# Kernel tuning notes

Hardware: AMD Instinct MI355X
Metric: run time of the kernel (lower is better)

Reference implementation:

```python
import jax, jax.numpy as jnp
import numpy as np

NEG_INF = -1e9


def setup_inputs() -> dict:
    key = jax.random.key(0)
    k1, k2, k3, k4, k5, k6 = jax.random.split(key, 6)
    B, P, N, C, H = 32, 512, 64, 9, 128
    polylines = jax.random.normal(k1, (B, P, N, C), dtype=jnp.float32)
    polylines_mask = jax.random.uniform(k2, (B, P, N)) > 0.1
    # MLP params (Linear(C,H) -> ReLU -> Linear(H,H)), torch-style init scale
    W1 = jax.random.uniform(k3, (C, H), minval=-1.0, maxval=1.0) / jnp.sqrt(C)
    b1 = jax.random.uniform(k4, (H,), minval=-1.0, maxval=1.0) / jnp.sqrt(C)
    W2 = jax.random.uniform(k5, (H, H), minval=-1.0, maxval=1.0) / jnp.sqrt(H)
    b2 = jax.random.uniform(k6, (H,), minval=-1.0, maxval=1.0) / jnp.sqrt(H)
    return {"polylines": polylines, "polylines_mask": polylines_mask,
            "W1": W1, "b1": b1, "W2": W2, "b2": b2}


def reference(polylines, polylines_mask, W1, b1, W2, b2):
    # Point MLP applied to all points (invalid ones are overwritten below,
    # identical math to the torch masked-gather version).
    h = jax.nn.relu(jnp.einsum('bpnc,ch->bpnh', polylines, W1) + b1)
    feat = jnp.einsum('bpnh,hd->bpnd', h, W2) + b2  # [B,P,N,H]
    feat = jnp.where(polylines_mask[..., None], feat, NEG_INF)
    pooled = jnp.max(feat, axis=2)  # [B,P,H]
    # Polylines with no valid points pooled to NEG_INF -> zero them out.
    any_valid = jnp.any(polylines_mask, axis=2)  # [B,P]
    return jnp.where(any_valid[..., None], pooled, 0.0)
```

## Files before the change

### kernel.cpp

```cpp
#include <hip/hip_runtime.h>


using bf16x8 = __attribute__((ext_vector_type(8))) short;
using f32x4  = __attribute__((ext_vector_type(4))) float;

#define MFMA32(A,B,C) __builtin_amdgcn_mfma_f32_16x16x32_bf16((A),(B),(C),0,0,0)

__device__ __forceinline__ f32x4 vmax4(f32x4 a, f32x4 b) {
  return __builtin_elementwise_max(a, b);
}

__device__ __forceinline__ unsigned short f2bf(float f) {
  union { float f; unsigned int u; } v; v.f = f;
  unsigned int r = v.u + 0x7fffu + ((v.u >> 16) & 1u);
  return (unsigned short)(r >> 16);
}

__device__ __forceinline__ unsigned int pack_bf2(float a, float b) {
  union { float f; unsigned int u; } ua, ub; ua.f = a; ub.f = b;
  return __builtin_amdgcn_perm(ub.u + 0x8000u, ua.u + 0x8000u, 0x07060302u);
}

__global__ void prep1(const float* __restrict__ W1, const float* __restrict__ W2,
                      const void* __restrict__ mask,
                      unsigned short* __restrict__ w1sw, unsigned short* __restrict__ w2sw,
                      int* __restrict__ flag) {
  int b = blockIdx.x, t = threadIdx.x;
  if (b == 0) {
    __shared__ int cnt;
    if (t == 0) cnt = 0;
    __syncthreads();
    const unsigned char* mb = (const unsigned char*)mask;
    int local = 0;
    for (int i = t * 16; i < t * 16 + 16; i++) local += (mb[i] != 0) ? 1 : 0;
    atomicAdd(&cnt, local);
    __syncthreads();
    if (t == 0) *flag = (cnt > 2800) ? 1 : 0;
  } else if (b <= 2) {
    int e = (b - 1) * 256 + t;
    int lane = e & 63, grp = e >> 6;
    int li = lane & 15, q = lane >> 4;
    int h = grp * 16 + li;
    int c0 = q * 8;
    #pragma unroll
    for (int j = 0; j < 8; j++) {
      int c = c0 + j;
      w1sw[e * 8 + j] = f2bf((c < 9) ? W1[c * 128 + h] : 0.f);
    }
  } else {
    int e = (b - 3) * 256 + t;
    if (e < 2048) {
      int lane = e & 63, grp = e >> 6;
      int wr = grp >> 4, sub = grp & 15;
      int ks = sub >> 2, td = sub & 3;
      int li = lane & 15, q = lane >> 4;
      int d = wr * 64 + td * 16 + li;
      int h0 = ks * 32 + q * 8;
      #pragma unroll
      for (int j = 0; j < 8; j++)
        w2sw[e * 8 + j] = f2bf(W2[(h0 + j) * 128 + d]);
    }
  }
}

__global__ __launch_bounds__(256, 4) void poly_main_k(
    const float* __restrict__ X, const void* __restrict__ mask,
    const float* __restrict__ b1g, const float* __restrict__ b2g,
    const unsigned short* __restrict__ w1sw, const unsigned short* __restrict__ w2sw,
    const int* __restrict__ flagp, float* __restrict__ out)
{
  __shared__ __align__(16) unsigned char smem[32768];
  float*          Xs = (float*)smem;
  unsigned short* Hb = (unsigned short*)smem;
  float*          P  = (float*)smem;

  const int tid  = threadIdx.x;
  const int lane = tid & 63;
  const int w    = tid >> 6;
  const int wr   = w >> 1, wc = w & 1;
  const int li   = lane & 15, q = lane >> 4;

  float mf[4];
  {
    int flag = *flagp;
    long long mb = (long long)blockIdx.x * 128 + wc * 64 + li;
    if (flag) {
      const unsigned char* mp = (const unsigned char*)mask;
      #pragma unroll
      for (int tm = 0; tm < 4; tm++) mf[tm] = mp[mb + tm * 16] ? 0.f : -4e9f;
    } else {
      const int* mp = (const int*)mask;
      #pragma unroll
      for (int tm = 0; tm < 4; tm++) mf[tm] = mp[mb + tm * 16] ? 0.f : -4e9f;
    }
  }

  {
    const f32x4* xg = (const f32x4*)(X + (long long)blockIdx.x * 1152);
    f32x4* xl = (f32x4*)Xs;
    xl[tid] = xg[tid];
    if (tid < 32) xl[tid + 256] = xg[tid + 256];
  }
  __syncthreads();

  bf16x8 bx[4];
  #pragma unroll
  for (int tm = 0; tm < 4; tm++) {
    int m = wc * 64 + tm * 16 + li;
    const float* xr = Xs + m * 9;
    union { bf16x8 v; unsigned int u[4]; } uu;
    uu.u[0] = uu.u[1] = uu.u[2] = uu.u[3] = 0u;
    if (q == 0) {
      uu.u[0] = pack_bf2(xr[0], xr[1]); uu.u[1] = pack_bf2(xr[2], xr[3]);
      uu.u[2] = pack_bf2(xr[4], xr[5]); uu.u[3] = pack_bf2(xr[6], xr[7]);
    } else if (q == 1) {
      uu.u[0] = pack_bf2(xr[8], 0.f);
    }
    bx[tm] = uu.v;
  }
  __syncthreads();

  #pragma unroll
  for (int th = 0; th < 4; th++) {
    bf16x8 a1 = *(const bf16x8*)(w1sw + ((wr * 4 + th) * 64 + lane) * 8);
    f32x4 bv = *(const f32x4*)(b1g + wr * 64 + th * 16 + q * 4);
    f32x4 acc[4];
    #pragma unroll
    for (int tm = 0; tm < 4; tm++) acc[tm] = bv;
    #pragma unroll
    for (int tm = 0; tm < 4; tm++) acc[tm] = MFMA32(a1, bx[tm], acc[tm]);
    #pragma unroll
    for (int tm = 0; tm < 4; tm++) {
      int m = wc * 64 + tm * 16 + li;
      f32x4 v = vmax4(acc[tm], f32x4{0.f, 0.f, 0.f, 0.f});
      uint2 hv;
      hv.x = pack_bf2(v[0], v[1]);
      hv.y = pack_bf2(v[2], v[3]);
      int chunk = (wr * 8 + th * 2 + (q >> 1)) ^ li;
      *(uint2*)(Hb + m * 128 + chunk * 8 + (q & 1) * 4) = hv;
    }
  }
  __syncthreads();

  f32x4 pooled[4];
  #pragma unroll
  for (int tm = 0; tm < 4; tm++) {
    int m = wc * 64 + tm * 16 + li;
    f32x4 acc[4];
    #pragma unroll
    for (int td = 0; td < 4; td++) acc[td] = f32x4{0.f, 0.f, 0.f, 0.f};
    #pragma unroll
    for (int ks = 0; ks < 4; ks++) {
      int chunk = (ks * 4 + q) ^ li;
      bf16x8 bb = *(const bf16x8*)(Hb + m * 128 + chunk * 8);
      #pragma unroll
      for (int td = 0; td < 4; td++) {
        bf16x8 a2 = *(const bf16x8*)(w2sw + (((wr * 16 + ks * 4 + td) * 64) + lane) * 8);
        acc[td] = MFMA32(a2, bb, acc[td]);
      }
    }
    if (tm == 0) {
      #pragma unroll
      for (int td = 0; td < 4; td++) pooled[td] = acc[td] + mf[0];
    } else {
      #pragma unroll
      for (int td = 0; td < 4; td++) pooled[td] = vmax4(pooled[td], acc[td] + mf[tm]);
    }
  }
  #pragma unroll
  for (int td = 0; td < 4; td++)
    pooled[td] += *(const f32x4*)(b2g + wr * 64 + td * 16 + q * 4);

  __syncthreads();
  #pragma unroll
  for (int td = 0; td < 4; td++)
    *(f32x4*)(P + (wc * 16 + li) * 132 + wr * 64 + td * 16 + q * 4) = pooled[td];
  __syncthreads();

  {
    int p = tid >> 7, d = tid & 127;
    const float* Pp = P + p * (16 * 132) + d;
    float v = Pp[0];
    #pragma unroll
    for (int j = 1; j < 16; j++) v = fmaxf(v, Pp[j * 132]);
    if (v < -1e8f) v = 0.f;
    out[(long long)blockIdx.x * 256 + tid] = v;
  }
}

extern "C" void kernel_launch(void* const* d_in, const int* in_sizes, int n_in,
                              void* d_out, int out_size, void* d_ws, size_t ws_size,
                              hipStream_t stream) {
  const float* X    = (const float*)d_in[0];
  const void*  mask = d_in[1];
  const float* W1   = (const float*)d_in[2];
  const float* b1   = (const float*)d_in[3];
  const float* W2   = (const float*)d_in[4];
  const float* b2   = (const float*)d_in[5];
  float* out = (float*)d_out;

  unsigned short* w1sw = (unsigned short*)d_ws;
  unsigned short* w2sw = (unsigned short*)((char*)d_ws + 8192);
  int* flag            = (int*)((char*)d_ws + 40960);

  prep1<<<11, 256, 0, stream>>>(W1, W2, mask, w1sw, w2sw, flag);
  poly_main_k<<<8192, 256, 0, stream>>>(X, mask, b1, b2, w1sw, w2sw, flag, out);
}
```

Before: 138.9 us.

## Switch second GEMM to 32x32 MFMA with mask folded into augmented K column

The second layer now uses 32x32x16 bf16 MFMA with points as the M dimension. K is extended to 144, and an extra column holding 1.0 for invalid points, multiplied by a weight row of -4e9, folds the mask penalty into the GEMM. Max-pooling happens inside each wave's accumulator, with a lane shuffle and a much smaller shared reduction at the end. The price is 9 K-steps instead of 8 (about 12% more MFMA work), a padded LDS row stride of 146 elements, and an extra prep block to build the new W2 layout.

```diff
diff --git a/kernel.cpp b/kernel.cpp
--- a/kernel.cpp
+++ b/kernel.cpp
@@ -3,8 +3,10 @@
 
 using bf16x8 = __attribute__((ext_vector_type(8))) short;
 using f32x4  = __attribute__((ext_vector_type(4))) float;
-
-#define MFMA32(A,B,C) __builtin_amdgcn_mfma_f32_16x16x32_bf16((A),(B),(C),0,0,0)
+using f32x16 = __attribute__((ext_vector_type(16))) float;
+
+#define MFMA16x16(A,B,C) __builtin_amdgcn_mfma_f32_16x16x32_bf16((A),(B),(C),0,0,0)
+#define MFMA32x32(A,B,C) __builtin_amdgcn_mfma_f32_32x32x16_bf16((A),(B),(C),0,0,0)
 
 __device__ __forceinline__ f32x4 vmax4(f32x4 a, f32x4 b) {
   return __builtin_elementwise_max(a, b);
@@ -49,16 +51,17 @@
     }
   } else {
     int e = (b - 3) * 256 + t;
-    if (e < 2048) {
+    if (e < 2304) {
       int lane = e & 63, grp = e >> 6;
-      int wr = grp >> 4, sub = grp & 15;
-      int ks = sub >> 2, td = sub & 3;
-      int li = lane & 15, q = lane >> 4;
-      int d = wr * 64 + td * 16 + li;
-      int h0 = ks * 32 + q * 8;
+      int dt = grp / 9, kb = grp - dt * 9;
+      int d = dt * 32 + (lane & 31);
+      int k0 = kb * 16 + (lane >> 5) * 8;
       #pragma unroll
-      for (int j = 0; j < 8; j++)
-        w2sw[e * 8 + j] = f2bf(W2[(h0 + j) * 128 + d]);
+      for (int j = 0; j < 8; j++) {
+        int k = k0 + j;
+        float v = (k < 128) ? W2[k * 128 + d] : ((k == 128) ? -4e9f : 0.f);
+        w2sw[e * 8 + j] = f2bf(v);
+      }
     }
   }
 }
@@ -69,9 +72,9 @@
     const unsigned short* __restrict__ w1sw, const unsigned short* __restrict__ w2sw,
     const int* __restrict__ flagp, float* __restrict__ out)
 {
-  __shared__ __align__(16) unsigned char smem[32768];
+  __shared__ __align__(16) unsigned char smem[128 * 146 * 2];
   float*          Xs = (float*)smem;
-  unsigned short* Hb = (unsigned short*)smem;
+  unsigned short* Hs = (unsigned short*)smem;
   float*          P  = (float*)smem;
 
   const int tid  = threadIdx.x;
@@ -79,21 +82,6 @@
   const int w    = tid >> 6;
   const int wr   = w >> 1, wc = w & 1;
   const int li   = lane & 15, q = lane >> 4;
-
-  float mf[4];
-  {
-    int flag = *flagp;
-    long long mb = (long long)blockIdx.x * 128 + wc * 64 + li;
-    if (flag) {
-      const unsigned char* mp = (const unsigned char*)mask;
-      #pragma unroll
-      for (int tm = 0; tm < 4; tm++) mf[tm] = mp[mb + tm * 16] ? 0.f : -4e9f;
-    } else {
-      const int* mp = (const int*)mask;
-      #pragma unroll
-      for (int tm = 0; tm < 4; tm++) mf[tm] = mp[mb + tm * 16] ? 0.f : -4e9f;
-    }
-  }
 
   {
     const f32x4* xg = (const f32x4*)(X + (long long)blockIdx.x * 1152);
@@ -128,7 +116,7 @@
     #pragma unroll
     for (int tm = 0; tm < 4; tm++) acc[tm] = bv;
     #pragma unroll
-    for (int tm = 0; tm < 4; tm++) acc[tm] = MFMA32(a1, bx[tm], acc[tm]);
+    for (int tm = 0; tm < 4; tm++) acc[tm] = MFMA16x16(a1, bx[tm], acc[tm]);
     #pragma unroll
     for (int tm = 0; tm < 4; tm++) {
       int m = wc * 64 + tm * 16 + li;
@@ -136,53 +124,58 @@
       uint2 hv;
       hv.x = pack_bf2(v[0], v[1]);
       hv.y = pack_bf2(v[2], v[3]);
-      int chunk = (wr * 8 + th * 2 + (q >> 1)) ^ li;
-      *(uint2*)(Hb + m * 128 + chunk * 8 + (q & 1) * 4) = hv;
-    }
-  }
-  __syncthreads();
-
-  f32x4 pooled[4];
-  #pragma unroll
-  for (int tm = 0; tm < 4; tm++) {
-    int m = wc * 64 + tm * 16 + li;
-    f32x4 acc[4];
-    #pragma unroll
-    for (int td = 0; td < 4; td++) acc[td] = f32x4{0.f, 0.f, 0.f, 0.f};
-    #pragma unroll
-    for (int ks = 0; ks < 4; ks++) {
-      int chunk = (ks * 4 + q) ^ li;
-      bf16x8 bb = *(const bf16x8*)(Hb + m * 128 + chunk * 8);
+      *(uint2*)(Hs + m * 146 + wr * 64 + th * 16 + q * 4) = hv;
+    }
+  }
+
+  {
+    int flag = *flagp;
+    int m2 = tid >> 1, half = tid & 1;
+    long long gi = (long long)blockIdx.x * 128 + m2;
+    unsigned int ind = 0u;
+    if (half == 0) {
+      bool valid = flag ? (((const unsigned char*)mask)[gi] != 0)
+                        : (((const int*)mask)[gi] != 0);
+      ind = valid ? 0u : 0x00003F80u;
+    }
+    unsigned int* dst = (unsigned int*)(Hs + m2 * 146 + 128) + half * 4;
+    dst[0] = ind; dst[1] = 0u; dst[2] = 0u; dst[3] = 0u;
+  }
+  __syncthreads();
+
+  float pool[4];
+  {
+    const unsigned short* abase = Hs + (w * 32 + (lane & 31)) * 146 + (lane >> 5) * 8;
+    #pragma unroll
+    for (int dt = 0; dt < 4; dt++) {
+      f32x16 acc = {0.f};
       #pragma unroll
-      for (int td = 0; td < 4; td++) {
-        bf16x8 a2 = *(const bf16x8*)(w2sw + (((wr * 16 + ks * 4 + td) * 64) + lane) * 8);
-        acc[td] = MFMA32(a2, bb, acc[td]);
+      for (int kb = 0; kb < 9; kb++) {
+        bf16x8 af = *(const bf16x8*)(abase + kb * 16);
+        bf16x8 bf = *(const bf16x8*)(w2sw + ((dt * 9 + kb) * 64 + lane) * 8);
+        acc = MFMA32x32(af, bf, acc);
       }
-    }
-    if (tm == 0) {
-      #pragma unroll
-      for (int td = 0; td < 4; td++) pooled[td] = acc[td] + mf[0];
-    } else {
-      #pragma unroll
-      for (int td = 0; td < 4; td++) pooled[td] = vmax4(pooled[td], acc[td] + mf[tm]);
-    }
-  }
-  #pragma unroll
-  for (int td = 0; td < 4; td++)
-    pooled[td] += *(const f32x4*)(b2g + wr * 64 + td * 16 + q * 4);
-
-  __syncthreads();
-  #pragma unroll
-  for (int td = 0; td < 4; td++)
-    *(f32x4*)(P + (wc * 16 + li) * 132 + wr * 64 + td * 16 + q * 4) = pooled[td];
+      float p0 = fmaxf(fmaxf(acc[0],  acc[1]),  fmaxf(acc[2],  acc[3]));
+      float p1 = fmaxf(fmaxf(acc[4],  acc[5]),  fmaxf(acc[6],  acc[7]));
+      float p2 = fmaxf(fmaxf(acc[8],  acc[9]),  fmaxf(acc[10], acc[11]));
+      float p3 = fmaxf(fmaxf(acc[12], acc[13]), fmaxf(acc[14], acc[15]));
+      float pm = fmaxf(fmaxf(p0, p1), fmaxf(p2, p3));
+      pm = fmaxf(pm, __shfl_xor(pm, 32, 64));
+      pool[dt] = pm + b2g[dt * 32 + (lane & 31)];
+    }
+  }
+
+  __syncthreads();
+  if (lane < 32) {
+    #pragma unroll
+    for (int dt = 0; dt < 4; dt++)
+      P[w * 128 + dt * 32 + lane] = pool[dt];
+  }
   __syncthreads();
 
   {
     int p = tid >> 7, d = tid & 127;
-    const float* Pp = P + p * (16 * 132) + d;
-    float v = Pp[0];
-    #pragma unroll
-    for (int j = 1; j < 16; j++) v = fmaxf(v, Pp[j * 132]);
+    float v = fmaxf(P[(2 * p) * 128 + d], P[(2 * p + 1) * 128 + d]);
     if (v < -1e8f) v = 0.f;
     out[(long long)blockIdx.x * 256 + tid] = v;
   }
@@ -201,8 +194,8 @@
 
   unsigned short* w1sw = (unsigned short*)d_ws;
   unsigned short* w2sw = (unsigned short*)((char*)d_ws + 8192);
-  int* flag            = (int*)((char*)d_ws + 40960);
-
-  prep1<<<11, 256, 0, stream>>>(W1, W2, mask, w1sw, w2sw, flag);
+  int* flag            = (int*)((char*)d_ws + 45056);
+
+  prep1<<<12, 256, 0, stream>>>(W1, W2, mask, w1sw, w2sw, flag);
   poly_main_k<<<8192, 256, 0, stream>>>(X, mask, b1, b2, w1sw, w2sw, flag, out);
 }
```

New measurement: 196.4 us. 1.41x slower.

## Make blocks persistent over four tiles with register-prefetched double-buffered input

Applied to the files above, without the earlier changes.

The grid shrinks from 8192 to 2048 blocks, and each block loops over four tiles strided by 2048. The next tile's X and mask are loaded into registers while the current tile's MFMAs run, then stored into the other half of a double-buffered LDS array. The final pooling now uses wave shuffles instead of a shared-memory transpose plus extra barriers. This aims to hide global load latency and cut block launch and sync overhead, at the cost of more LDS (about 41KB) and registers, which may lower occupancy.

```diff
diff --git a/kernel.cpp b/kernel.cpp
--- a/kernel.cpp
+++ b/kernel.cpp
@@ -69,122 +69,166 @@
     const unsigned short* __restrict__ w1sw, const unsigned short* __restrict__ w2sw,
     const int* __restrict__ flagp, float* __restrict__ out)
 {
-  __shared__ __align__(16) unsigned char smem[32768];
-  float*          Xs = (float*)smem;
-  unsigned short* Hb = (unsigned short*)smem;
-  float*          P  = (float*)smem;
+  __shared__ __align__(16) float Xs[2][1152];
+  __shared__ __align__(16) unsigned short Hb[128 * 128];
 
   const int tid  = threadIdx.x;
   const int lane = tid & 63;
   const int w    = tid >> 6;
   const int wr   = w >> 1, wc = w & 1;
   const int li   = lane & 15, q = lane >> 4;
-
-  float mf[4];
+  const int flag = *flagp;
+
+  const unsigned char* mp8  = (const unsigned char*)mask;
+  const int*           mp32 = (const int*)mask;
+
+  long long tile = blockIdx.x;
+  f32x4 xa, xb;
+  unsigned int mcur[4];
   {
-    int flag = *flagp;
-    long long mb = (long long)blockIdx.x * 128 + wc * 64 + li;
+    const f32x4* xg = (const f32x4*)(X + tile * 1152);
+    xa = xg[tid];
+    int i2 = tid + 256; if (i2 > 287) i2 = 287;
+    xb = xg[i2];
+    long long mb = tile * 128 + wc * 64 + li;
     if (flag) {
-      const unsigned char* mp = (const unsigned char*)mask;
-      #pragma unroll
-      for (int tm = 0; tm < 4; tm++) mf[tm] = mp[mb + tm * 16] ? 0.f : -4e9f;
+      #pragma unroll
+      for (int tm = 0; tm < 4; tm++) mcur[tm] = mp8[mb + tm * 16];
     } else {
-      const int* mp = (const int*)mask;
-      #pragma unroll
-      for (int tm = 0; tm < 4; tm++) mf[tm] = mp[mb + tm * 16] ? 0.f : -4e9f;
-    }
-  }
-
+      #pragma unroll
+      for (int tm = 0; tm < 4; tm++) mcur[tm] = (unsigned int)mp32[mb + tm * 16];
+    }
+  }
   {
-    const f32x4* xg = (const f32x4*)(X + (long long)blockIdx.x * 1152);
-    f32x4* xl = (f32x4*)Xs;
-    xl[tid] = xg[tid];
-    if (tid < 32) xl[tid + 256] = xg[tid + 256];
-  }
-  __syncthreads();
-
-  bf16x8 bx[4];
+    f32x4* xl = (f32x4*)Xs[0];
+    xl[tid] = xa;
+    if (tid < 32) xl[tid + 256] = xb;
+  }
+
   #pragma unroll
-  for (int tm = 0; tm < 4; tm++) {
-    int m = wc * 64 + tm * 16 + li;
-    const float* xr = Xs + m * 9;
-    union { bf16x8 v; unsigned int u[4]; } uu;
-    uu.u[0] = uu.u[1] = uu.u[2] = uu.u[3] = 0u;
-    if (q == 0) {
-      uu.u[0] = pack_bf2(xr[0], xr[1]); uu.u[1] = pack_bf2(xr[2], xr[3]);
-      uu.u[2] = pack_bf2(xr[4], xr[5]); uu.u[3] = pack_bf2(xr[6], xr[7]);
-    } else if (q == 1) {
-      uu.u[0] = pack_bf2(xr[8], 0.f);
-    }
-    bx[tm] = uu.v;
-  }
-  __syncthreads();
-
-  #pragma unroll
-  for (int th = 0; th < 4; th++) {
-    bf16x8 a1 = *(const bf16x8*)(w1sw + ((wr * 4 + th) * 64 + lane) * 8);
-    f32x4 bv = *(const f32x4*)(b1g + wr * 64 + th * 16 + q * 4);
-    f32x4 acc[4];
-    #pragma unroll
-    for (int tm = 0; tm < 4; tm++) acc[tm] = bv;
-    #pragma unroll
-    for (int tm = 0; tm < 4; tm++) acc[tm] = MFMA32(a1, bx[tm], acc[tm]);
+  for (int it = 0; it < 4; it++) {
+    const int cur = it & 1;
+    __syncthreads();
+
+    float mf[4];
+    #pragma unroll
+    for (int tm = 0; tm < 4; tm++) mf[tm] = mcur[tm] ? 0.f : -4e9f;
+
+    bf16x8 bx[4];
     #pragma unroll
     for (int tm = 0; tm < 4; tm++) {
       int m = wc * 64 + tm * 16 + li;
-      f32x4 v = vmax4(acc[tm], f32x4{0.f, 0.f, 0.f, 0.f});
-      uint2 hv;
-      hv.x = pack_bf2(v[0], v[1]);
-      hv.y = pack_bf2(v[2], v[3]);
-      int chunk = (wr * 8 + th * 2 + (q >> 1)) ^ li;
-      *(uint2*)(Hb + m * 128 + chunk * 8 + (q & 1) * 4) = hv;
-    }
-  }
-  __syncthreads();
-
-  f32x4 pooled[4];
-  #pragma unroll
-  for (int tm = 0; tm < 4; tm++) {
-    int m = wc * 64 + tm * 16 + li;
-    f32x4 acc[4];
-    #pragma unroll
-    for (int td = 0; td < 4; td++) acc[td] = f32x4{0.f, 0.f, 0.f, 0.f};
-    #pragma unroll
-    for (int ks = 0; ks < 4; ks++) {
-      int chunk = (ks * 4 + q) ^ li;
-      bf16x8 bb = *(const bf16x8*)(Hb + m * 128 + chunk * 8);
+      const float* xr = Xs[cur] + m * 9;
+      union { bf16x8 v; unsigned int u[4]; } uu;
+      uu.u[0] = uu.u[1] = uu.u[2] = uu.u[3] = 0u;
+      if (q == 0) {
+        uu.u[0] = pack_bf2(xr[0], xr[1]); uu.u[1] = pack_bf2(xr[2], xr[3]);
+        uu.u[2] = pack_bf2(xr[4], xr[5]); uu.u[3] = pack_bf2(xr[6], xr[7]);
+      } else if (q == 1) {
+        uu.u[0] = pack_bf2(xr[8], 0.f);
+      }
+      bx[tm] = uu.v;
+    }
+
+    long long ntile = (long long)blockIdx.x + (long long)((it < 3) ? (it + 1) : it) * 2048;
+    f32x4 xa2, xb2;
+    unsigned int mnext[4];
+    {
+      const f32x4* xg2 = (const f32x4*)(X + ntile * 1152);
+      xa2 = xg2[tid];
+      int i2 = tid + 256; if (i2 > 287) i2 = 287;
+      xb2 = xg2[i2];
+      long long mb2 = ntile * 128 + wc * 64 + li;
+      if (flag) {
+        #pragma unroll
+        for (int tm = 0; tm < 4; tm++) mnext[tm] = mp8[mb2 + tm * 16];
+      } else {
+        #pragma unroll
+        for (int tm = 0; tm < 4; tm++) mnext[tm] = (unsigned int)mp32[mb2 + tm * 16];
+      }
+    }
+
+    #pragma unroll
+    for (int th = 0; th < 4; th++) {
+      bf16x8 a1 = *(const bf16x8*)(w1sw + ((wr * 4 + th) * 64 + lane) * 8);
+      f32x4 bv = *(const f32x4*)(b1g + wr * 64 + th * 16 + q * 4);
+      f32x4 acc[4];
+      #pragma unroll
+      for (int tm = 0; tm < 4; tm++) acc[tm] = bv;
+      #pragma unroll
+      for (int tm = 0; tm < 4; tm++) acc[tm] = MFMA32(a1, bx[tm], acc[tm]);
+      #pragma unroll
+      for (int tm = 0; tm < 4; tm++) {
+        int m = wc * 64 + tm * 16 + li;
+        f32x4 v = vmax4(acc[tm], f32x4{0.f, 0.f, 0.f, 0.f});
+        uint2 hv;
+        hv.x = pack_bf2(v[0], v[1]);
+        hv.y = pack_bf2(v[2], v[3]);
+        int chunk = (wr * 8 + th * 2 + (q >> 1)) ^ li;
+        *(uint2*)(Hb + m * 128 + chunk * 8 + (q & 1) * 4) = hv;
+      }
+    }
+    __syncthreads();
+
+    f32x4 pooled[4];
+    #pragma unroll
+    for (int tm = 0; tm < 4; tm++) {
+      int m = wc * 64 + tm * 16 + li;
+      f32x4 acc[4];
+      #pragma unroll
+      for (int td = 0; td < 4; td++) acc[td] = f32x4{0.f, 0.f, 0.f, 0.f};
+      #pragma unroll
+      for (int ks = 0; ks < 4; ks++) {
+        int chunk = (ks * 4 + q) ^ li;
+        bf16x8 bb = *(const bf16x8*)(Hb + m * 128 + chunk * 8);
+        #pragma unroll
+        for (int td = 0; td < 4; td++) {
+          bf16x8 a2 = *(const bf16x8*)(w2sw + (((wr * 16 + ks * 4 + td) * 64) + lane) * 8);
+          acc[td] = MFMA32(a2, bb, acc[td]);
+        }
+      }
+      if (tm == 0) {
+        #pragma unroll
+        for (int td = 0; td < 4; td++) pooled[td] = acc[td] + mf[0];
+      } else {
+        #pragma unroll
+        for (int td = 0; td < 4; td++) pooled[td] = vmax4(pooled[td], acc[td] + mf[tm]);
+      }
+    }
+    #pragma unroll
+    for (int td = 0; td < 4; td++)
+      pooled[td] += *(const f32x4*)(b2g + wr * 64 + td * 16 + q * 4);
+
+    #pragma unroll
+    for (int s = 8; s >= 1; s >>= 1) {
       #pragma unroll
       for (int td = 0; td < 4; td++) {
-        bf16x8 a2 = *(const bf16x8*)(w2sw + (((wr * 16 + ks * 4 + td) * 64) + lane) * 8);
-        acc[td] = MFMA32(a2, bb, acc[td]);
-      }
-    }
-    if (tm == 0) {
-      #pragma unroll
-      for (int td = 0; td < 4; td++) pooled[td] = acc[td] + mf[0];
-    } else {
-      #pragma unroll
-      for (int td = 0; td < 4; td++) pooled[td] = vmax4(pooled[td], acc[td] + mf[tm]);
-    }
-  }
-  #pragma unroll
-  for (int td = 0; td < 4; td++)
-    pooled[td] += *(const f32x4*)(b2g + wr * 64 + td * 16 + q * 4);
-
-  __syncthreads();
-  #pragma unroll
-  for (int td = 0; td < 4; td++)
-    *(f32x4*)(P + (wc * 16 + li) * 132 + wr * 64 + td * 16 + q * 4) = pooled[td];
-  __syncthreads();
-
-  {
-    int p = tid >> 7, d = tid & 127;
-    const float* Pp = P + p * (16 * 132) + d;
-    float v = Pp[0];
-    #pragma unroll
-    for (int j = 1; j < 16; j++) v = fmaxf(v, Pp[j * 132]);
-    if (v < -1e8f) v = 0.f;
-    out[(long long)blockIdx.x * 256 + tid] = v;
+        #pragma unroll
+        for (int r = 0; r < 4; r++) {
+          float o = __shfl_xor(pooled[td][r], s, 64);
+          pooled[td][r] = fmaxf(pooled[td][r], o);
+        }
+      }
+    }
+    if (li == 0) {
+      long long poly = tile * 2 + wc;
+      #pragma unroll
+      for (int td = 0; td < 4; td++) {
+        f32x4 v = pooled[td];
+        #pragma unroll
+        for (int r = 0; r < 4; r++) if (v[r] < -1e8f) v[r] = 0.f;
+        *(f32x4*)(out + poly * 128 + wr * 64 + td * 16 + q * 4) = v;
+      }
+    }
+
+    {
+      f32x4* xl = (f32x4*)Xs[cur ^ 1];
+      xl[tid] = xa2;
+      if (tid < 32) xl[tid + 256] = xb2;
+    }
+    #pragma unroll
+    for (int tm = 0; tm < 4; tm++) mcur[tm] = mnext[tm];
+    tile = ntile;
   }
 }
 
@@ -204,5 +248,5 @@
   int* flag            = (int*)((char*)d_ws + 40960);
 
   prep1<<<11, 256, 0, stream>>>(W1, W2, mask, w1sw, w2sw, flag);
-  poly_main_k<<<8192, 256, 0, stream>>>(X, mask, b1, b2, w1sw, w2sw, flag, out);
-}
+  poly_main_k<<<2048, 256, 0, stream>>>(X, mask, b1, b2, w1sw, w2sw, flag, out);
+}
```

New measurement: 169.4 us. +21.9%, slower.
